# Optimization experiments

Hardware: AMD Instinct MI355X
Metric: run time of the kernel (lower is better)

The kernel has to match this reference:

```python
import jax, jax.numpy as jnp
import numpy as np

CHEB_K = 3  # diffusion_steps

def setup_inputs() -> dict:
    key = jax.random.key(0)
    k1, k2, k3 = jax.random.split(key, 3)
    N, D, B, C, O, K = 2048, 16, 64, 64, 64, CHEB_K
    node_embeddings = jax.random.normal(k1, (N, D), dtype=jnp.float32)
    feat = jax.random.normal(k2, (B, N, C), dtype=jnp.float32)
    # kaiming-uniform-like init for weights_pool, zeros bias (matches reset_parameters)
    fan_in = K * C  # fan_in of [D, K, C, O] per torch convention (dims after first)
    bound = 1.0 / np.sqrt(fan_in)
    weights_pool = jax.random.uniform(k3, (D, K, C, O), dtype=jnp.float32,
                                      minval=-bound, maxval=bound)
    bias_pool = jnp.zeros((D, O), dtype=jnp.float32)
    return {"node_embeddings": node_embeddings, "feat": feat,
            "weights_pool": weights_pool, "bias_pool": bias_pool}

def reference(node_embeddings, feat, weights_pool, bias_pool):
    N = node_embeddings.shape[0]
    K = weights_pool.shape[1]
    # adaptive adjacency: softmax(relu(E E^T)) row-wise
    sim = node_embeddings @ node_embeddings.T            # [N, N]
    supports = jax.nn.softmax(jax.nn.relu(sim), axis=1)  # [N, N]
    # Chebyshev polynomial recurrence: T0=I, T1=A, Tk = 2A Tk-1 - Tk-2
    support_set = [jnp.eye(N, dtype=supports.dtype), supports]
    for _ in range(2, K):
        support_set.append(2.0 * supports @ support_set[-1] - support_set[-2])
    supports_k = jnp.stack(support_set, axis=0)          # [K, N, N]
    # node-conditioned weights and bias
    weights = jnp.einsum('nd,dkio->nkio', node_embeddings, weights_pool)  # [N,K,C,O]
    bias = node_embeddings @ bias_pool                                    # [N, O]
    # graph diffusion of features
    x_g = jnp.einsum('knm,bmc->bknc', supports_k, feat)  # [B, K, N, C]
    x_g = jnp.transpose(x_g, (0, 2, 1, 3))               # [B, N, K, C]
    # per-node batched GEMM + bias
    x_gconv = jnp.einsum('bnki,nkio->bno', x_g, weights) + bias
    return x_gconv
```

## Files before the change

### kernel.cpp

```cpp
#include <hip/hip_runtime.h>
#include <stdint.h>

#define NN 2048
#define DE 16
#define BB 64
#define CC 64
#define OO 64
#define BC 4096
#define KR 192
#define JJ 12288

using bf16x8 = __attribute__((ext_vector_type(8))) __bf16;
using f32x4  = __attribute__((ext_vector_type(4))) float;

__device__ __forceinline__ unsigned short f2bf(float f) {
  union { float f; unsigned int u; } v; v.f = f;
  unsigned int u = v.u;
  return (unsigned short)((u + 0x7FFFu + ((u >> 16) & 1u)) >> 16);
}
__device__ __forceinline__ float bf2f(unsigned short h) {
  union { unsigned int u; float f; } v; v.u = ((unsigned int)h) << 16;
  return v.f;
}
__device__ __forceinline__ void gll16(const void* g, void* l) {
  __builtin_amdgcn_global_load_lds(
      (const __attribute__((address_space(1))) unsigned int*)g,
      (__attribute__((address_space(3))) unsigned int*)l, 16, 0, 0);
}

__global__ __launch_bounds__(256) void prep(const float* __restrict__ feat,
                                            const float* __restrict__ E,
                                            const float* __restrict__ wp,
                                            const float* __restrict__ bp,
                                            unsigned short* __restrict__ Fbf,
                                            unsigned short* __restrict__ FbfT,
                                            unsigned short* __restrict__ Abf,
                                            float* __restrict__ Bias,
                                            unsigned short* __restrict__ Ebf,
                                            unsigned short* __restrict__ wpT2) {
  __shared__ float smem[64 * 65];
  const int id = blockIdx.x;
  const int t  = threadIdx.x;

  if (id < 2048) {
    float (*tile)[65] = (float (*)[65])smem;
    const int b  = id >> 5;
    const int n0 = (id & 31) * 64;
    const int tr = t >> 4, tc4 = (t & 15) * 4;
#pragma unroll
    for (int i = 0; i < 4; ++i) {
      const int r = tr + i * 16;
      const float4 v = *(const float4*)(feat + (size_t)b * (NN * CC) + (size_t)(n0 + r) * CC + tc4);
      tile[r][tc4 + 0] = v.x; tile[r][tc4 + 1] = v.y;
      tile[r][tc4 + 2] = v.z; tile[r][tc4 + 3] = v.w;
    }
    __syncthreads();
#pragma unroll
    for (int i = 0; i < 4; ++i) {
      const int r = tr + i * 16;
      const unsigned int lo = f2bf(tile[r][tc4 + 0]) | ((unsigned int)f2bf(tile[r][tc4 + 1]) << 16);
      const unsigned int hi = f2bf(tile[r][tc4 + 2]) | ((unsigned int)f2bf(tile[r][tc4 + 3]) << 16);
      *(uint2*)(Fbf + (size_t)(n0 + r) * BC + b * CC + tc4) = make_uint2(lo, hi);
    }
#pragma unroll
    for (int u = 0; u < 4; ++u) {
      const int p = t + u * 256;
      const int c = p >> 4, n4 = (p & 15) * 4;
      const unsigned int lo = f2bf(tile[n4 + 0][c]) | ((unsigned int)f2bf(tile[n4 + 1][c]) << 16);
      const unsigned int hi = f2bf(tile[n4 + 2][c]) | ((unsigned int)f2bf(tile[n4 + 3][c]) << 16);
      *(uint2*)(FbfT + (size_t)(b * CC + c) * NN + n0 + n4) = make_uint2(lo, hi);
    }
  } else if (id < 2560) {
    const int n0base = (id - 2048) * 4;
    float* esm  = smem;
    float* redm = smem + 64;
    float* reds = smem + 80;
    if (t < 64) esm[t] = E[n0base * 16 + t];
    __syncthreads();
    if (t < 64) Ebf[n0base * 16 + t] = f2bf(esm[t]);
    float er[4][16];
#pragma unroll
    for (int rr = 0; rr < 4; ++rr)
#pragma unroll
      for (int d = 0; d < 16; ++d) er[rr][d] = esm[rr * 16 + d];

    float v[8][4];
    float mx[4] = {0.f, 0.f, 0.f, 0.f};
#pragma unroll
    for (int i = 0; i < 8; ++i) {
      const int m = t + i * 256;
      const float4* Em = (const float4*)(E + m * 16);
      const float4 a = Em[0], b = Em[1], c = Em[2], d = Em[3];
#pragma unroll
      for (int rr = 0; rr < 4; ++rr) {
        float dot = er[rr][0] * a.x + er[rr][1] * a.y + er[rr][2] * a.z + er[rr][3] * a.w
                  + er[rr][4] * b.x + er[rr][5] * b.y + er[rr][6] * b.z + er[rr][7] * b.w
                  + er[rr][8] * c.x + er[rr][9] * c.y + er[rr][10] * c.z + er[rr][11] * c.w
                  + er[rr][12] * d.x + er[rr][13] * d.y + er[rr][14] * d.z + er[rr][15] * d.w;
        const float r = fmaxf(dot, 0.0f);
        v[i][rr] = r;
        mx[rr] = fmaxf(mx[rr], r);
      }
    }
    const int wave = t >> 6, lane = t & 63;
#pragma unroll
    for (int rr = 0; rr < 4; ++rr) {
#pragma unroll
      for (int off = 32; off > 0; off >>= 1) mx[rr] = fmaxf(mx[rr], __shfl_xor(mx[rr], off, 64));
      if (lane == 0) redm[wave * 4 + rr] = mx[rr];
    }
    __syncthreads();
#pragma unroll
    for (int rr = 0; rr < 4; ++rr)
      mx[rr] = fmaxf(fmaxf(redm[rr], redm[4 + rr]), fmaxf(redm[8 + rr], redm[12 + rr]));
    float s[4] = {0.f, 0.f, 0.f, 0.f};
#pragma unroll
    for (int i = 0; i < 8; ++i)
#pragma unroll
      for (int rr = 0; rr < 4; ++rr) { v[i][rr] = __expf(v[i][rr] - mx[rr]); s[rr] += v[i][rr]; }
#pragma unroll
    for (int rr = 0; rr < 4; ++rr) {
#pragma unroll
      for (int off = 32; off > 0; off >>= 1) s[rr] += __shfl_xor(s[rr], off, 64);
      if (lane == 0) reds[wave * 4 + rr] = s[rr];
    }
    __syncthreads();
    float inv[4];
#pragma unroll
    for (int rr = 0; rr < 4; ++rr)
      inv[rr] = 1.0f / (reds[rr] + reds[4 + rr] + reds[8 + rr] + reds[12 + rr]);
#pragma unroll
    for (int i = 0; i < 8; ++i)
#pragma unroll
      for (int rr = 0; rr < 4; ++rr)
        Abf[(size_t)(n0base + rr) * NN + t + i * 256] = f2bf(v[i][rr] * inv[rr]);
    if (t < 64) {
#pragma unroll
      for (int rr = 0; rr < 4; ++rr) {
        float bs = 0.0f;
#pragma unroll
        for (int d = 0; d < 16; ++d) bs += esm[rr * 16 + d] * bp[d * 64 + t];
        Bias[(size_t)(n0base + rr) * 64 + t] = bs;
      }
    }
  } else {
    const int rq = id - 2560;
    for (int p = t; p < 1024; p += 256) {
      const int e0 = p * 8;
      const int d0 = e0 & 15;
      const int rem = e0 >> 4;
      const int rl = rem & 7, o = rem >> 3;
      const int r = rq * 8 + rl;
      unsigned int w[4];
#pragma unroll
      for (int u = 0; u < 4; ++u) {
        const float f0 = wp[(size_t)(d0 + 2 * u) * JJ + r * 64 + o];
        const float f1 = wp[(size_t)(d0 + 2 * u + 1) * JJ + r * 64 + o];
        w[u] = f2bf(f0) | ((unsigned int)f2bf(f1) << 16);
      }
      *(uint4*)(wpT2 + (size_t)rq * 8192 + e0) = make_uint4(w[0], w[1], w[2], w[3]);
    }
  }
}

template <int EPI>
__global__ __launch_bounds__(256, 6) void gemm_mw(const unsigned short* __restrict__ A,
                                                  const unsigned short* __restrict__ Bt,
                                                  unsigned short* __restrict__ Cnm,
                                                  unsigned short* __restrict__ Ct,
                                                  const unsigned short* __restrict__ F,
                                                  const unsigned short* __restrict__ Ebf,
                                                  const unsigned short* __restrict__ wpT2,
                                                  unsigned short* __restrict__ Wg,
                                                  int mwbase) {
  __shared__ alignas(16) unsigned short As[128 * 64];
  __shared__ alignas(16) unsigned short Bs[64 * 64];
  const int id = blockIdx.x;
  const int t = threadIdx.x;
  const int wave = t >> 6, lane = t & 63;
  const int li = lane & 15, q = lane >> 4;

  if (id >= 1024) {
    const int wid = id - 1024 + mwbase;
    const int bj = (wid % 96) * 128;
    const int bm = (wid / 96) * 128;
    gll16(Ebf  + (size_t)(bm + (t >> 1)) * 16 + (t & 1) * 8, &As[t * 8]);
    gll16(wpT2 + (size_t)(bj + (t >> 1)) * 16 + (t & 1) * 8, &Bs[t * 8]);
    __syncthreads();
    const int wm = (wave >> 1) * 64, wj = (wave & 1) * 64;
    const bool hiK = (q >= 2);
    const int qq = q & 1;
    bf16x8 vz;
#pragma unroll
    for (int i = 0; i < 8; ++i) vz[i] = (__bf16)0.0f;
    bf16x8 af[4], bfr[4];
#pragma unroll
    for (int r = 0; r < 4; ++r) {
      af[r] = *(const bf16x8*)&As[(wm + r * 16 + li) * 16 + qq * 8];
      if (hiK) af[r] = vz;
    }
#pragma unroll
    for (int c = 0; c < 4; ++c) {
      bfr[c] = *(const bf16x8*)&Bs[(wj + c * 16 + li) * 16 + qq * 8];
      if (hiK) bfr[c] = vz;
    }
    const int rowL = q * 4;
#pragma unroll
    for (int r = 0; r < 4; ++r) {
#pragma unroll
      for (int c = 0; c < 4; ++c) {
        f32x4 acc = (f32x4){0.f, 0.f, 0.f, 0.f};
        acc = __builtin_amdgcn_mfma_f32_16x16x32_bf16(af[r], bfr[c], acc, 0, 0, 0);
        const int gm = bm + wm + r * 16 + rowL;
        const int gj = bj + wj + c * 16 + li;
#pragma unroll
        for (int i = 0; i < 4; ++i)
          Wg[(size_t)(gm + i) * JJ + gj] = f2bf(acc[i]);
      }
    }
    return;
  }

  const int bm = (id >> 6) * 128, bn = (id & 63) * 64;
  const int wm = wave * 32;

  f32x4 acc[2][4];
#pragma unroll
  for (int r = 0; r < 2; ++r)
#pragma unroll
    for (int c = 0; c < 4; ++c) acc[r][c] = (f32x4){0.f, 0.f, 0.f, 0.f};

  const int srow = t >> 3;
  const int csw = (((t & 7) ^ ((t >> 4) & 7)) * 8);
  const unsigned short* Ap[4];
  const unsigned short* Bp[2];
#pragma unroll
  for (int i = 0; i < 4; ++i) Ap[i] = A + (size_t)(bm + srow + i * 32) * NN + csw;
#pragma unroll
  for (int i = 0; i < 2; ++i) Bp[i] = Bt + (size_t)(bn + srow + i * 32) * NN + csw;
  const int sw = (li >> 1) & 7;

  for (int k0 = 0; k0 < NN; k0 += 64) {
    __syncthreads();
#pragma unroll
    for (int i = 0; i < 4; ++i) gll16(Ap[i] + k0, &As[(t + i * 256) * 8]);
#pragma unroll
    for (int i = 0; i < 2; ++i) gll16(Bp[i] + k0, &Bs[(t + i * 256) * 8]);
    __syncthreads();
#pragma unroll
    for (int kk = 0; kk < 2; ++kk) {
      const int kc = ((kk * 4 + q) ^ sw) * 8;
      bf16x8 af[2], bfr[4];
#pragma unroll
      for (int r = 0; r < 2; ++r)
        af[r] = *(const bf16x8*)&As[(wm + r * 16 + li) * 64 + kc];
#pragma unroll
      for (int c = 0; c < 4; ++c)
        bfr[c] = *(const bf16x8*)&Bs[(c * 16 + li) * 64 + kc];
#pragma unroll
      for (int r = 0; r < 2; ++r)
#pragma unroll
        for (int c = 0; c < 4; ++c)
          acc[r][c] = __builtin_amdgcn_mfma_f32_16x16x32_bf16(af[r], bfr[c], acc[r][c], 0, 0, 0);
    }
  }

  const int rowL = q * 4;
#pragma unroll
  for (int r = 0; r < 2; ++r) {
#pragma unroll
    for (int c = 0; c < 4; ++c) {
      const int gm = bm + wm + r * 16 + rowL;
      const int gn = bn + c * 16 + li;
      const f32x4 a = acc[r][c];
      if (EPI == 1) {
#pragma unroll
        for (int i = 0; i < 4; ++i)
          Cnm[(size_t)(gm + i) * BC + gn] = f2bf(a[i]);
        const unsigned int lo = f2bf(a[0]) | ((unsigned int)f2bf(a[1]) << 16);
        const unsigned int hi = f2bf(a[2]) | ((unsigned int)f2bf(a[3]) << 16);
        *(uint2*)(Ct + (size_t)gn * NN + gm) = make_uint2(lo, hi);
      } else {
#pragma unroll
        for (int i = 0; i < 4; ++i) {
          const float g = 2.0f * a[i] - bf2f(F[(size_t)(gm + i) * BC + gn]);
          Cnm[(size_t)(gm + i) * BC + gn] = f2bf(g);
        }
      }
    }
  }
}

__global__ __launch_bounds__(256, 6) void final_gemm(const unsigned short* __restrict__ Fbf,
                                                     const unsigned short* __restrict__ G1,
                                                     const unsigned short* __restrict__ G2,
                                                     const unsigned short* __restrict__ Wg,
                                                     const float* __restrict__ Bias,
                                                     float* __restrict__ out) {
  const int n = blockIdx.x, t = threadIdx.x;
  const int wave = t >> 6, lane = t & 63;
  const int li = lane & 15, q = lane >> 4;
  const unsigned short* xb[3] = {Fbf + (size_t)n * BC + (size_t)(wave * 16 + li) * 64,
                                 G1  + (size_t)n * BC + (size_t)(wave * 16 + li) * 64,
                                 G2  + (size_t)n * BC + (size_t)(wave * 16 + li) * 64};
  const unsigned short* wb = Wg + (size_t)n * JJ + (size_t)q * 512 + li * 8;

  f32x4 acc[4];
#pragma unroll
  for (int c = 0; c < 4; ++c) acc[c] = (f32x4){0.f, 0.f, 0.f, 0.f};
#pragma unroll
  for (int kq = 0; kq < 6; ++kq) {
    const bf16x8 a = *(const bf16x8*)(xb[kq >> 1] + (kq & 1) * 32 + q * 8);
#pragma unroll
    for (int c = 0; c < 4; ++c) {
      const bf16x8 b = *(const bf16x8*)(wb + (size_t)kq * 2048 + c * 128);
      acc[c] = __builtin_amdgcn_mfma_f32_16x16x32_bf16(a, b, acc[c], 0, 0, 0);
    }
  }
  const int rbase = wave * 16 + q * 4;
#pragma unroll
  for (int c = 0; c < 4; ++c) {
    const int o = c * 16 + li;
    const float bs = Bias[n * 64 + o];
#pragma unroll
    for (int i = 0; i < 4; ++i)
      out[(size_t)(rbase + i) * (NN * OO) + (size_t)n * OO + o] = acc[c][i] + bs;
  }
}

extern "C" void kernel_launch(void* const* d_in, const int* in_sizes, int n_in,
                              void* d_out, int out_size, void* d_ws, size_t ws_size,
                              hipStream_t stream) {
  const float* E    = (const float*)d_in[0];
  const float* feat = (const float*)d_in[1];
  const float* wp   = (const float*)d_in[2];
  const float* bp   = (const float*)d_in[3];
  float* out = (float*)d_out;

  char* ws = (char*)d_ws;
  size_t off = 0;
  auto alloc = [&](size_t bytes) -> void* {
    void* p = ws + off;
    off += (bytes + 255) & ~(size_t)255;
    return p;
  };
  unsigned short* Abf  = (unsigned short*)alloc((size_t)NN * NN * 2);
  unsigned short* FbfT = (unsigned short*)alloc((size_t)BC * NN * 2);
  unsigned short* Fbf  = (unsigned short*)alloc((size_t)NN * BC * 2);
  unsigned short* G1   = (unsigned short*)alloc((size_t)NN * BC * 2);
  unsigned short* G1T  = (unsigned short*)alloc((size_t)BC * NN * 2);
  unsigned short* Wg   = (unsigned short*)alloc((size_t)NN * JJ * 2);
  float* Bias          = (float*)alloc((size_t)NN * OO * 4);
  unsigned short* Ebf  = (unsigned short*)alloc((size_t)NN * DE * 2);
  unsigned short* wpT2 = (unsigned short*)alloc((size_t)JJ * DE * 2);
  unsigned short* G2   = FbfT;

  prep<<<dim3(2584), 256, 0, stream>>>(feat, E, wp, bp, Fbf, FbfT, Abf, Bias, Ebf, wpT2);
  gemm_mw<1><<<dim3(1792), 256, 0, stream>>>(Abf, FbfT, G1, G1T, nullptr, Ebf, wpT2, Wg, 0);
  gemm_mw<2><<<dim3(1792), 256, 0, stream>>>(Abf, G1T, G2, nullptr, Fbf, Ebf, wpT2, Wg, 768);
  final_gemm<<<dim3(2048), 256, 0, stream>>>(Fbf, G1, G2, Wg, Bias, out);
}
```

Baseline: 262.8 us.

## Fold Chebyshev recurrence into weights instead of second-hop epilogue

Rewrites T2 = 2A·T1 - I so the second diffusion GEMM outputs plain H = A·G1 and the combination is absorbed into the node weights: W0' = W0 - W2 and W2' = 2·W2, computed in the weight-pool prep. This removes the read of the bf16 features in the second GEMM epilogue and the fused subtract. It also lowers the gemm_mw occupancy hint from 6 to 4 and drops the bound on final_gemm. Rounding now happens on the modified weights rather than on T2·X, which slightly changes the numerics.

```diff
diff --git a/kernel.cpp b/kernel.cpp
--- a/kernel.cpp
+++ b/kernel.cpp
@@ -17,10 +17,6 @@
   union { float f; unsigned int u; } v; v.f = f;
   unsigned int u = v.u;
   return (unsigned short)((u + 0x7FFFu + ((u >> 16) & 1u)) >> 16);
-}
-__device__ __forceinline__ float bf2f(unsigned short h) {
-  union { unsigned int u; float f; } v; v.u = ((unsigned int)h) << 16;
-  return v.f;
 }
 __device__ __forceinline__ void gll16(const void* g, void* l) {
   __builtin_amdgcn_global_load_lds(
@@ -154,8 +150,15 @@
       unsigned int w[4];
 #pragma unroll
       for (int u = 0; u < 4; ++u) {
-        const float f0 = wp[(size_t)(d0 + 2 * u) * JJ + r * 64 + o];
-        const float f1 = wp[(size_t)(d0 + 2 * u + 1) * JJ + r * 64 + o];
+        float f0 = wp[(size_t)(d0 + 2 * u) * JJ + r * 64 + o];
+        float f1 = wp[(size_t)(d0 + 2 * u + 1) * JJ + r * 64 + o];
+        if (rq < 8) {
+          f0 -= wp[(size_t)(d0 + 2 * u) * JJ + (r + 128) * 64 + o];
+          f1 -= wp[(size_t)(d0 + 2 * u + 1) * JJ + (r + 128) * 64 + o];
+        } else if (rq >= 16) {
+          f0 *= 2.0f;
+          f1 *= 2.0f;
+        }
         w[u] = f2bf(f0) | ((unsigned int)f2bf(f1) << 16);
       }
       *(uint4*)(wpT2 + (size_t)rq * 8192 + e0) = make_uint4(w[0], w[1], w[2], w[3]);
@@ -164,11 +167,10 @@
 }
 
 template <int EPI>
-__global__ __launch_bounds__(256, 6) void gemm_mw(const unsigned short* __restrict__ A,
+__global__ __launch_bounds__(256, 4) void gemm_mw(const unsigned short* __restrict__ A,
                                                   const unsigned short* __restrict__ Bt,
                                                   unsigned short* __restrict__ Cnm,
                                                   unsigned short* __restrict__ Ct,
-                                                  const unsigned short* __restrict__ F,
                                                   const unsigned short* __restrict__ Ebf,
                                                   const unsigned short* __restrict__ wpT2,
                                                   unsigned short* __restrict__ Wg,
@@ -273,36 +275,30 @@
       const int gm = bm + wm + r * 16 + rowL;
       const int gn = bn + c * 16 + li;
       const f32x4 a = acc[r][c];
+#pragma unroll
+      for (int i = 0; i < 4; ++i)
+        Cnm[(size_t)(gm + i) * BC + gn] = f2bf(a[i]);
       if (EPI == 1) {
-#pragma unroll
-        for (int i = 0; i < 4; ++i)
-          Cnm[(size_t)(gm + i) * BC + gn] = f2bf(a[i]);
         const unsigned int lo = f2bf(a[0]) | ((unsigned int)f2bf(a[1]) << 16);
         const unsigned int hi = f2bf(a[2]) | ((unsigned int)f2bf(a[3]) << 16);
         *(uint2*)(Ct + (size_t)gn * NN + gm) = make_uint2(lo, hi);
-      } else {
-#pragma unroll
-        for (int i = 0; i < 4; ++i) {
-          const float g = 2.0f * a[i] - bf2f(F[(size_t)(gm + i) * BC + gn]);
-          Cnm[(size_t)(gm + i) * BC + gn] = f2bf(g);
-        }
-      }
-    }
-  }
-}
-
-__global__ __launch_bounds__(256, 6) void final_gemm(const unsigned short* __restrict__ Fbf,
-                                                     const unsigned short* __restrict__ G1,
-                                                     const unsigned short* __restrict__ G2,
-                                                     const unsigned short* __restrict__ Wg,
-                                                     const float* __restrict__ Bias,
-                                                     float* __restrict__ out) {
+      }
+    }
+  }
+}
+
+__global__ __launch_bounds__(256) void final_gemm(const unsigned short* __restrict__ Fbf,
+                                                  const unsigned short* __restrict__ G1,
+                                                  const unsigned short* __restrict__ H,
+                                                  const unsigned short* __restrict__ Wg,
+                                                  const float* __restrict__ Bias,
+                                                  float* __restrict__ out) {
   const int n = blockIdx.x, t = threadIdx.x;
   const int wave = t >> 6, lane = t & 63;
   const int li = lane & 15, q = lane >> 4;
   const unsigned short* xb[3] = {Fbf + (size_t)n * BC + (size_t)(wave * 16 + li) * 64,
                                  G1  + (size_t)n * BC + (size_t)(wave * 16 + li) * 64,
-                                 G2  + (size_t)n * BC + (size_t)(wave * 16 + li) * 64};
+                                 H   + (size_t)n * BC + (size_t)(wave * 16 + li) * 64};
   const unsigned short* wb = Wg + (size_t)n * JJ + (size_t)q * 512 + li * 8;
 
   f32x4 acc[4];
@@ -353,10 +349,10 @@
   float* Bias          = (float*)alloc((size_t)NN * OO * 4);
   unsigned short* Ebf  = (unsigned short*)alloc((size_t)NN * DE * 2);
   unsigned short* wpT2 = (unsigned short*)alloc((size_t)JJ * DE * 2);
-  unsigned short* G2   = FbfT;
+  unsigned short* H    = FbfT;
 
   prep<<<dim3(2584), 256, 0, stream>>>(feat, E, wp, bp, Fbf, FbfT, Abf, Bias, Ebf, wpT2);
-  gemm_mw<1><<<dim3(1792), 256, 0, stream>>>(Abf, FbfT, G1, G1T, nullptr, Ebf, wpT2, Wg, 0);
-  gemm_mw<2><<<dim3(1792), 256, 0, stream>>>(Abf, G1T, G2, nullptr, Fbf, Ebf, wpT2, Wg, 768);
-  final_gemm<<<dim3(2048), 256, 0, stream>>>(Fbf, G1, G2, Wg, Bias, out);
-}
+  gemm_mw<1><<<dim3(1792), 256, 0, stream>>>(Abf, FbfT, G1, G1T, Ebf, wpT2, Wg, 0);
+  gemm_mw<2><<<dim3(1792), 256, 0, stream>>>(Abf, G1T, H, nullptr, Ebf, wpT2, Wg, 768);
+  final_gemm<<<dim3(2048), 256, 0, stream>>>(Fbf, G1, H, Wg, Bias, out);
+}
```

Result: faster. 219.7 us (-16.4%).
